# Performance work log

Hardware: AMD Instinct MI355X
Metric: run time of the kernel (lower is better)

Reference implementation:

```python
import jax, jax.numpy as jnp
import numpy as np

B, C_IN, H, W = 4, 64, 384, 384
C_OUT, KER, R = 64, 3, 4
N = B * H * W


def _conv(x, w):
    # NCHW conv, stride 1, SAME padding (ker//2 for odd kernels)
    return jax.lax.conv_general_dilated(
        x, w, window_strides=(1, 1), padding='SAME',
        dimension_numbers=('NCHW', 'OIHW', 'NCHW'))


def setup_inputs() -> dict:
    key = jax.random.key(0)
    kx, kp, k1, k2, k3 = jax.random.split(key, 5)
    x = jax.random.normal(kx, (B, C_IN, H, W), dtype=jnp.float32)
    # disjoint partition of all b*h*w pixel indices
    perm = jax.random.permutation(kp, N)
    mask_idx = perm[: N // 2].astype(jnp.int32)
    inv_mask_idx = perm[N // 2:].astype(jnp.int32)
    # weights, init per the torch module: std = sqrt(2 / (out_channels * kH*kW))
    std_high = np.sqrt(2.0 / (C_OUT * KER * KER)).astype(np.float32)
    std_low1 = np.sqrt(2.0 / ((C_OUT // R) * KER * KER)).astype(np.float32)
    std_low2 = np.sqrt(2.0 / (C_OUT * 1 * 1)).astype(np.float32)
    high_w = jax.random.normal(k1, (C_OUT, C_IN, KER, KER), dtype=jnp.float32) * std_high
    low1_w = jax.random.normal(k2, (C_OUT // R, C_IN, KER, KER), dtype=jnp.float32) * std_low1
    low2_w = jax.random.normal(k3, (C_OUT, C_OUT // R, 1, 1), dtype=jnp.float32) * std_low2
    return {"x": x, "high_w": high_w, "low1_w": low1_w, "low2_w": low2_w,
            "mask_idx": mask_idx, "inv_mask_idx": inv_mask_idx}


def reference(x, high_w, low1_w, low2_w, mask_idx, inv_mask_idx):
    # eval_forward: per-pixel routed conv (no bias on either path).
    # Pixels in mask_idx get the full 3x3 conv; pixels in inv_mask_idx get the
    # low-rank bottleneck path (3x3 conv to C/r, then 1x1 conv back to C).
    b, c, h, w = x.shape
    n = b * h * w
    high = _conv(x, high_w)                     # (b, cout, h, w)
    low = _conv(_conv(x, low1_w), low2_w)       # (b, cout, h, w)
    # flatten to pixel-major order matching torch's b*h*w flattening
    hf = high.transpose(0, 2, 3, 1).reshape(n, -1)  # (n, cout)
    lf = low.transpose(0, 2, 3, 1).reshape(n, -1)
    is_high = jnp.zeros((n,), dtype=bool).at[mask_idx].set(True)
    yf = jnp.where(is_high[:, None], hf, lf)
    return yf.reshape(b, h, w, -1).transpose(0, 3, 1, 2)
```

## Files before the change

### kernel.cpp

```cpp
#include <hip/hip_runtime.h>
#include <hip/hip_bf16.h>
#include <stdint.h>

typedef __attribute__((ext_vector_type(8))) short  short8;
typedef __attribute__((ext_vector_type(4))) float  float4_t;
typedef __attribute__((ext_vector_type(4))) int    int4_t;

constexpr int BB = 4, CIN = 64, COUT = 64, HH = 384, WW = 384;
constexpr int HWc  = HH * WW;
constexpr int NPIX = BB * HWc;
constexpr int TR = 12, TC = 32;
constexpr int SR = TR + 2, SC = TC + 2;
constexpr int NGRP = SR * SC * 8;

__device__ __forceinline__ unsigned short f2bf(float f) {
    unsigned u = __builtin_bit_cast(unsigned, f);
    unsigned r = u + 0x7FFFu + ((u >> 16) & 1u);
    return (unsigned short)(r >> 16);
}

__global__ void k_flags(const int* __restrict__ mi, const int* __restrict__ ii,
                        unsigned char* __restrict__ flags, int half) {
    int i = blockIdx.x * blockDim.x + threadIdx.x;
    if (i < half) { flags[mi[i]] = 1; flags[ii[i]] = 0; }
}

__global__ void k_wpack(const float* __restrict__ hw_, const float* __restrict__ l1w,
                        const float* __restrict__ l2w,
                        unsigned short* __restrict__ Wp, unsigned short* __restrict__ Ap2) {
    int i = blockIdx.x * 256 + threadIdx.x;
    if (i < 18 * 5 * 64) {
        int lane = i & 63, tile = (i >> 6) % 5, chunk = i / 320;
        int tap = chunk >> 1, h = chunk & 1, ky = tap / 3, kx = tap % 3;
        int m = lane & 15, quad = lane >> 4;
        for (int j = 0; j < 8; j++) {
            int cin = h * 32 + quad * 8 + j;
            float wv;
            if (tile < 4) { int co = tile * 16 + m; wv = hw_[((co * 64 + cin) * 3 + ky) * 3 + kx]; }
            else          { wv = l1w[((m * 64 + cin) * 3 + ky) * 3 + kx]; }
            Wp[(size_t)i * 8 + j] = f2bf(wv);
        }
    }
    if (i < 4 * 64) {
        int lane = i & 63, tile = i >> 6;
        int m = lane & 15, quad = lane >> 4;
        for (int j = 0; j < 8; j++) {
            unsigned short v = 0;
            if (j < 4) { int c = quad * 4 + j; v = f2bf(l2w[(tile * 16 + m) * 16 + c]); }
            Ap2[(size_t)i * 8 + j] = v;
        }
    }
}

__global__ __launch_bounds__(256, 2) void k_main(
    const float* __restrict__ x,
    const unsigned short* __restrict__ Wp,
    const unsigned short* __restrict__ Ap2,
    const unsigned char* __restrict__ flags,
    float* __restrict__ out)
{
    __shared__ __align__(16) unsigned short X[SR * SC * 64];

    const int tid = threadIdx.x;
    const int x0  = blockIdx.x * TC;
    const int y0  = blockIdx.y * TR;
    const int b   = blockIdx.z;

    const float* xb = x + (size_t)b * CIN * HWc;
#pragma unroll 1
    for (int s = tid; s < NGRP; s += 256) {
        int q   = s / (SR * SC);
        int p   = s - q * (SR * SC);
        int row = p / SC;
        int col = p - row * SC;
        int gy  = y0 + row - 1;
        int gx  = x0 + col - 1;
        bool ok = ((unsigned)gy < (unsigned)HH) && ((unsigned)gx < (unsigned)WW);
        int off = ok ? (gy * WW + gx) : 0;
        const float* xp = xb + (size_t)(q * 8) * HWc + off;
        unsigned pk[4];
#pragma unroll
        for (int jj = 0; jj < 4; jj++) {
            float f0 = xp[(size_t)(2 * jj)     * HWc];
            float f1 = xp[(size_t)(2 * jj + 1) * HWc];
            if (!ok) { f0 = 0.f; f1 = 0.f; }
            pk[jj] = (unsigned)f2bf(f0) | ((unsigned)f2bf(f1) << 16);
        }
        int blk = q ^ (col & 7);
        *(int4_t*)&X[p * 64 + blk * 8] = *(int4_t*)pk;
    }
    __syncthreads();

    const int lane = tid & 63;
    const int w    = tid >> 6;
    const int n16  = lane & 15;
    const int quad = lane >> 4;

    float4_t acc[5][6];
#pragma unroll
    for (int t = 0; t < 5; t++)
#pragma unroll
        for (int f = 0; f < 6; f++) acc[t][f] = (float4_t)0.0f;

    const int4_t* wp4 = (const int4_t*)Wp;
    short8 a_cur[5], a_nxt[5];
#pragma unroll
    for (int t = 0; t < 5; t++)
        a_cur[t] = __builtin_bit_cast(short8, wp4[t * 64 + lane]);

#pragma unroll 1
    for (int chunk = 0; chunk < 18; chunk++) {
        if (chunk < 17) {
#pragma unroll
            for (int t = 0; t < 5; t++)
                a_nxt[t] = __builtin_bit_cast(short8, wp4[((chunk + 1) * 5 + t) * 64 + lane]);
        }
        const int tap = chunk >> 1, h = chunk & 1;
        const int ky = tap / 3, kx = tap % 3;
        short8 bf[6];
#pragma unroll
        for (int f = 0; f < 6; f++) {
            int idx = w * 6 + f;
            int r = idx >> 1, ch = idx & 1;
            int xh  = ch * 16 + n16 + kx;
            int blk = (h * 4 + quad) ^ (xh & 7);
            bf[f] = __builtin_bit_cast(short8,
                    *(const int4_t*)&X[((r + ky) * SC + xh) * 64 + blk * 8]);
        }
#pragma unroll
        for (int f = 0; f < 6; f++)
#pragma unroll
            for (int t = 0; t < 5; t++)
                acc[t][f] = __builtin_amdgcn_mfma_f32_16x16x32_bf16(a_cur[t], bf[f], acc[t][f], 0, 0, 0);
#pragma unroll
        for (int t = 0; t < 5; t++) a_cur[t] = a_nxt[t];
    }

    short8 a2[4];
    const int4_t* ap4 = (const int4_t*)Ap2;
#pragma unroll
    for (int t = 0; t < 4; t++)
        a2[t] = __builtin_bit_cast(short8, ap4[t * 64 + lane]);

#pragma unroll
    for (int f = 0; f < 6; f++) {
        int idx = w * 6 + f;
        int r = idx >> 1, ch = idx & 1;
        float4_t m4 = acc[4][f];
        short8 bfrag;
#pragma unroll
        for (int j = 0; j < 8; j++)
            bfrag[j] = (j < 4) ? (short)f2bf(m4[j]) : (short)0;

        int gy = y0 + r, gx = x0 + ch * 16 + n16;
        bool hiF = flags[b * HWc + gy * WW + gx] != 0;
        float* ob = out + (size_t)b * COUT * HWc + gy * WW + gx;
#pragma unroll
        for (int t = 0; t < 4; t++) {
            float4_t low = __builtin_amdgcn_mfma_f32_16x16x32_bf16(a2[t], bfrag, (float4_t)0.0f, 0, 0, 0);
            float4_t hi = acc[t][f];
#pragma unroll
            for (int i = 0; i < 4; i++) {
                int co = t * 16 + quad * 4 + i;
                ob[(size_t)co * HWc] = hiF ? hi[i] : low[i];
            }
        }
    }
}

extern "C" void kernel_launch(void* const* d_in, const int* in_sizes, int n_in,
                              void* d_out, int out_size, void* d_ws, size_t ws_size,
                              hipStream_t stream) {
    const float* x   = (const float*)d_in[0];
    const float* hw_ = (const float*)d_in[1];
    const float* l1w = (const float*)d_in[2];
    const float* l2w = (const float*)d_in[3];
    const int*   mi  = (const int*)d_in[4];
    const int*   ii  = (const int*)d_in[5];
    float*       out = (float*)d_out;

    unsigned char*  flags = (unsigned char*)d_ws;
    size_t off = (NPIX + 15) & ~(size_t)15;
    unsigned short* Wp    = (unsigned short*)((char*)d_ws + off); off += 18 * 5 * 64 * 8 * 2;
    unsigned short* Ap2   = (unsigned short*)((char*)d_ws + off);

    const int half = NPIX / 2;
    k_flags<<<(half + 255) / 256, 256, 0, stream>>>(mi, ii, flags, half);
    k_wpack<<<(18 * 5 * 64 + 255) / 256, 256, 0, stream>>>(hw_, l1w, l2w, Wp, Ap2);
    k_main<<<dim3(WW / TC, HH / TR, BB), 256, 0, stream>>>(x, Wp, Ap2, flags, out);
}
```

Measured before the change: 344.7 us.

## Vectorize halo tile loads with float4 and shrink tile for higher occupancy

The shared-memory staging loop now has each thread load four consecutive pixels per channel as float4 vectors, with a scalar fallback at image borders, instead of one scalar pixel per channel group. The tile height drops from 12 to 8 rows, so each wave holds fewer accumulators and launch bounds request 3 blocks per CU. This targets the cost of uncoalesced global loads during staging and aims to give more latency hiding. In exchange, the halo overhead per tile rises and the grid has more blocks.

```diff
diff --git a/kernel.cpp b/kernel.cpp
--- a/kernel.cpp
+++ b/kernel.cpp
@@ -9,9 +9,9 @@
 constexpr int BB = 4, CIN = 64, COUT = 64, HH = 384, WW = 384;
 constexpr int HWc  = HH * WW;
 constexpr int NPIX = BB * HWc;
-constexpr int TR = 12, TC = 32;
+constexpr int TR = 8, TC = 32;
 constexpr int SR = TR + 2, SC = TC + 2;
-constexpr int NGRP = SR * SC * 8;
+constexpr int NTASK = SR * 9 * 8;
 
 __device__ __forceinline__ unsigned short f2bf(float f) {
     unsigned u = __builtin_bit_cast(unsigned, f);
@@ -52,7 +52,7 @@
     }
 }
 
-__global__ __launch_bounds__(256, 2) void k_main(
+__global__ __launch_bounds__(256, 3) void k_main(
     const float* __restrict__ x,
     const unsigned short* __restrict__ Wp,
     const unsigned short* __restrict__ Ap2,
@@ -68,26 +68,41 @@
 
     const float* xb = x + (size_t)b * CIN * HWc;
 #pragma unroll 1
-    for (int s = tid; s < NGRP; s += 256) {
-        int q   = s / (SR * SC);
-        int p   = s - q * (SR * SC);
-        int row = p / SC;
-        int col = p - row * SC;
+    for (int t = tid; t < NTASK; t += 256) {
+        int g   = t % 9;
+        int q   = (t / 9) & 7;
+        int row = t / 72;
         int gy  = y0 + row - 1;
-        int gx  = x0 + col - 1;
-        bool ok = ((unsigned)gy < (unsigned)HH) && ((unsigned)gx < (unsigned)WW);
-        int off = ok ? (gy * WW + gx) : 0;
-        const float* xp = xb + (size_t)(q * 8) * HWc + off;
-        unsigned pk[4];
-#pragma unroll
-        for (int jj = 0; jj < 4; jj++) {
-            float f0 = xp[(size_t)(2 * jj)     * HWc];
-            float f1 = xp[(size_t)(2 * jj + 1) * HWc];
-            if (!ok) { f0 = 0.f; f1 = 0.f; }
-            pk[jj] = (unsigned)f2bf(f0) | ((unsigned)f2bf(f1) << 16);
-        }
-        int blk = q ^ (col & 7);
-        *(int4_t*)&X[p * 64 + blk * 8] = *(int4_t*)pk;
+        int gx0 = x0 - 1 + g * 4;
+        bool yok  = (unsigned)gy < (unsigned)HH;
+        bool fast = yok && (gx0 >= 0) && (gx0 <= WW - 4);
+        const float* xp = xb + (size_t)(q * 8) * HWc + gy * WW + gx0;
+        float4_t v[8];
+        if (fast) {
+#pragma unroll
+            for (int c = 0; c < 8; c++)
+                v[c] = *(const float4_t*)(xp + (size_t)c * HWc);
+        } else {
+#pragma unroll
+            for (int c = 0; c < 8; c++)
+#pragma unroll
+                for (int e = 0; e < 4; e++) {
+                    bool ok = yok && ((unsigned)(gx0 + e) < (unsigned)WW);
+                    v[c][e] = ok ? xp[(size_t)c * HWc + e] : 0.f;
+                }
+        }
+#pragma unroll
+        for (int e = 0; e < 4; e++) {
+            int col = g * 4 + e;
+            if (col < SC) {
+                unsigned pk[4];
+#pragma unroll
+                for (int jj = 0; jj < 4; jj++)
+                    pk[jj] = (unsigned)f2bf(v[2 * jj][e]) | ((unsigned)f2bf(v[2 * jj + 1][e]) << 16);
+                int blk = q ^ (col & 7);
+                *(int4_t*)&X[(row * SC + col) * 64 + blk * 8] = *(int4_t*)pk;
+            }
+        }
     }
     __syncthreads();
 
@@ -96,11 +111,11 @@
     const int n16  = lane & 15;
     const int quad = lane >> 4;
 
-    float4_t acc[5][6];
+    float4_t acc[5][4];
 #pragma unroll
     for (int t = 0; t < 5; t++)
 #pragma unroll
-        for (int f = 0; f < 6; f++) acc[t][f] = (float4_t)0.0f;
+        for (int f = 0; f < 4; f++) acc[t][f] = (float4_t)0.0f;
 
     const int4_t* wp4 = (const int4_t*)Wp;
     short8 a_cur[5], a_nxt[5];
@@ -117,18 +132,18 @@
         }
         const int tap = chunk >> 1, h = chunk & 1;
         const int ky = tap / 3, kx = tap % 3;
-        short8 bf[6];
-#pragma unroll
-        for (int f = 0; f < 6; f++) {
-            int idx = w * 6 + f;
-            int r = idx >> 1, ch = idx & 1;
+        short8 bf[4];
+#pragma unroll
+        for (int f = 0; f < 4; f++) {
+            int r  = 2 * w + (f >> 1);
+            int ch = f & 1;
             int xh  = ch * 16 + n16 + kx;
             int blk = (h * 4 + quad) ^ (xh & 7);
             bf[f] = __builtin_bit_cast(short8,
                     *(const int4_t*)&X[((r + ky) * SC + xh) * 64 + blk * 8]);
         }
 #pragma unroll
-        for (int f = 0; f < 6; f++)
+        for (int f = 0; f < 4; f++)
 #pragma unroll
             for (int t = 0; t < 5; t++)
                 acc[t][f] = __builtin_amdgcn_mfma_f32_16x16x32_bf16(a_cur[t], bf[f], acc[t][f], 0, 0, 0);
@@ -143,9 +158,9 @@
         a2[t] = __builtin_bit_cast(short8, ap4[t * 64 + lane]);
 
 #pragma unroll
-    for (int f = 0; f < 6; f++) {
-        int idx = w * 6 + f;
-        int r = idx >> 1, ch = idx & 1;
+    for (int f = 0; f < 4; f++) {
+        int r  = 2 * w + (f >> 1);
+        int ch = f & 1;
         float4_t m4 = acc[4][f];
         short8 bfrag;
 #pragma unroll
```

Result: faster. 328.7 us (-4.6%).
